# Performance work log

Hardware: AMD Instinct MI355X
Metric: run time of the kernel (lower is better)

Reference implementation:

```python
import jax, jax.numpy as jnp
import numpy as np

B = 512
IN_CORES = 12      # input_eff_capsules = 3072/256
N_PRIM = 12        # num_primary_capsules
N_PAR = 10         # num_parent_capsules
RFPC = 4           # receptive fields per capsule = 256/64
RF = 64            # receptive field size
CAP = 256          # capsule size
P_CONN = 0.2


def setup_inputs() -> dict:
    key = jax.random.key(0)
    ks = jax.random.split(key, 16)
    x = jax.random.uniform(ks[0], (B, 32, 32, 3), dtype=jnp.float32)
    # sparse 0/1 routing tensors (fixed Bernoulli(p) connectivity, stored as float params)
    C1 = jax.random.bernoulli(ks[1], P_CONN, (IN_CORES, RFPC, N_PRIM, RFPC)).astype(jnp.float32)
    C_skip = jax.random.bernoulli(ks[2], P_CONN, (IN_CORES, RFPC, N_PAR, RFPC)).astype(jnp.float32)
    C2 = jax.random.bernoulli(ks[3], P_CONN, (N_PRIM, RFPC, N_PAR, RFPC)).astype(jnp.float32)
    # per-receptive-field linear weights of the capsule layers
    s = 1.0 / np.sqrt(RF)
    W1 = jax.random.normal(ks[4], (N_PRIM, RFPC, RF, RF), dtype=jnp.float32) * s
    b1 = jnp.zeros((N_PRIM, RFPC, RF), dtype=jnp.float32)
    W2 = jax.random.normal(ks[5], (N_PAR, RFPC, RF, RF), dtype=jnp.float32) * s
    b2 = jnp.zeros((N_PAR, RFPC, RF), dtype=jnp.float32)
    # reconstruction MLP: 2560 -> 5000 -> 4000 -> 3072
    Wr1 = jax.random.normal(ks[6], (2560, 5000), dtype=jnp.float32) * (1.0 / np.sqrt(2560))
    br1 = jnp.zeros((5000,), dtype=jnp.float32)
    Wr2 = jax.random.normal(ks[7], (5000, 4000), dtype=jnp.float32) * (1.0 / np.sqrt(5000))
    br2 = jnp.zeros((4000,), dtype=jnp.float32)
    Wr3 = jax.random.normal(ks[8], (4000, 3072), dtype=jnp.float32) * (1.0 / np.sqrt(4000))
    br3 = jnp.zeros((3072,), dtype=jnp.float32)
    return {"x": x, "C1": C1, "W1": W1, "b1": b1, "C_skip": C_skip,
            "C2": C2, "W2": W2, "b2": b2,
            "Wr1": Wr1, "br1": br1, "Wr2": Wr2, "br2": br2, "Wr3": Wr3, "br3": br3}


def _caps_layer(x_flat, C, W, b):
    # x_flat: (B, in_cores*RFPC*RF); C: (in_cores, RFPC, out_caps, RFPC)
    bsz = x_flat.shape[0]
    in_cores = C.shape[0]
    xr = x_flat.reshape(bsz, in_cores, RFPC, RF)
    routed = jnp.einsum('ijkl,bijm->bklm', C, xr)          # (B, out_caps, RFPC, RF)
    out = jax.nn.relu(jnp.einsum('bklm,klmn->bkln', routed, W) + b)
    return out.reshape(bsz, -1)


def reference(x, C1, W1, b1, C_skip, C2, W2, b2, Wr1, br1, Wr2, br2, Wr3, br3):
    bsz = x.shape[0]
    # spatial_block_reshape: pure reshapes -> flatten
    x_flat = x.reshape(bsz, -1)                             # (B, 3072)
    # primary capsule layer
    x_prim = _caps_layer(x_flat, C1, W1, b1)                # (B, 3072)
    # skip connection: sparse routing einsum input->parent
    xr = x_prim.reshape(bsz, IN_CORES, RFPC, RF)
    x_skip = jnp.einsum('ijkl,bijm->bklm', C_skip, xr).reshape(bsz, -1)  # (B, 2560)
    # parent capsule layer + skip
    x_sum = x_skip + _caps_layer(x_prim, C2, W2, b2)        # (B, 2560)
    # top-1 capsule mask by norm
    norms = jnp.linalg.norm(x_sum.reshape(bsz, N_PAR, CAP), axis=-1)  # (B, 10)
    active = jnp.argmax(norms, axis=-1)                     # (B,)
    cap_id = jnp.arange(N_PAR * CAP) // CAP                 # (2560,)
    mask = (cap_id[None, :] == active[:, None]).astype(x_sum.dtype)
    x_recon = mask * x_sum
    # reconstruction MLP
    h = jax.nn.relu(x_recon @ Wr1 + br1)
    h = jax.nn.relu(h @ Wr2 + br2)
    out = jax.nn.sigmoid(h @ Wr3 + br3)                     # (B, 3072)
    return (out, x_sum)
```

## Files before the change

### kernel.cpp

```cpp
#include <hip/hip_runtime.h>
#include <math.h>


#define BATCH 512
#define OUT0_SZ (512*3072)

typedef __attribute__((ext_vector_type(8))) short short8;
typedef __attribute__((ext_vector_type(4))) float f32x4;

__device__ inline unsigned short f2bf(float f) {
    union { float f; unsigned u; } v; v.f = f;
    unsigned r = v.u + 0x7fffu + ((v.u >> 16) & 1u);
    return (unsigned short)(r >> 16);
}
__device__ inline float bf2f(unsigned int hi16) {
    union { unsigned u; float f; } v; v.u = hi16 << 16; return v.f;
}

#define GLD16(g, l) __builtin_amdgcn_global_load_lds( \
    (const __attribute__((address_space(1))) unsigned int*)(g), \
    (__attribute__((address_space(3))) unsigned int*)(l), 16, 0, 0)

struct CTJob {
    const float* W; unsigned short* Wt;
    int Kr, Nr, Kp, k0, n0;
};

__device__ inline CTJob ct_resolve(int bid,
    const float* Wr1, unsigned short* Wt1,
    const float* Wr2, unsigned short* Wt2,
    const float* Wr3, unsigned short* Wt3,
    const float* W1,  unsigned short* W1t,
    const float* W2,  unsigned short* W2t)
{
    CTJob j;
    int ktiles, rem;
    if (bid < 3200)       { j.W = Wr1; j.Wt = Wt1; j.Kr = 2560; j.Nr = 5000; j.Kp = 2560; ktiles = 40; rem = bid; }
    else if (bid < 8320)  { j.W = Wr2; j.Wt = Wt2; j.Kr = 5000; j.Nr = 4000; j.Kp = 5120; ktiles = 80; rem = bid - 3200; }
    else if (bid < 11392) { j.W = Wr3; j.Wt = Wt3; j.Kr = 4000; j.Nr = 3072; j.Kp = 4096; ktiles = 64; rem = bid - 8320; }
    else if (bid < 11440) { int kl = bid - 11392; j.W = W1 + (size_t)kl * 4096; j.Wt = W1t + (size_t)kl * 4096;
                            j.Kr = 64; j.Nr = 64; j.Kp = 64; ktiles = 1; rem = 0; }
    else                  { int kl = bid - 11440; j.W = W2 + (size_t)kl * 4096; j.Wt = W2t + (size_t)kl * 4096;
                            j.Kr = 64; j.Nr = 64; j.Kp = 64; ktiles = 1; rem = 0; }
    j.k0 = (rem % ktiles) * 64;
    j.n0 = (rem / ktiles) * 64;
    return j;
}

__device__ inline void ct_load(const CTJob& j, int tid, float4* v) {
    int kr = tid >> 4;
    int nc = (tid & 15) * 4;
    #pragma unroll
    for (int p = 0; p < 4; ++p) {
        int k = j.k0 + kr + p * 16;
        float4 vv = make_float4(0.f, 0.f, 0.f, 0.f);
        if (k < j.Kr) {
            if (j.n0 + nc + 3 < j.Nr) {
                vv = *(const float4*)&j.W[(size_t)k * j.Nr + j.n0 + nc];
            } else {
                float tmp[4] = {0.f, 0.f, 0.f, 0.f};
                #pragma unroll
                for (int jj = 0; jj < 4; ++jj)
                    if (j.n0 + nc + jj < j.Nr) tmp[jj] = j.W[(size_t)k * j.Nr + j.n0 + nc + jj];
                vv = make_float4(tmp[0], tmp[1], tmp[2], tmp[3]);
            }
        }
        v[p] = vv;
    }
}

__device__ inline void ct_stlds(float* t, int tid, const float4* v) {
    int kr = tid >> 4;
    int nc = (tid & 15) * 4;
    #pragma unroll
    for (int p = 0; p < 4; ++p) {
        float* row = &t[(kr + p * 16) * 65 + nc];
        row[0] = v[p].x; row[1] = v[p].y; row[2] = v[p].z; row[3] = v[p].w;
    }
}

__device__ inline void ct_pack(const CTJob& j, const float* t, int tid) {
    int nr = tid >> 2;
    int kc = (tid & 3) * 16;
    unsigned int u[8];
    #pragma unroll
    for (int jj = 0; jj < 8; ++jj) {
        float v0 = t[(kc + 2 * jj)     * 65 + nr];
        float v1 = t[(kc + 2 * jj + 1) * 65 + nr];
        u[jj] = (unsigned int)f2bf(v0) | ((unsigned int)f2bf(v1) << 16);
    }
    unsigned int* dst = (unsigned int*)&j.Wt[(size_t)(j.n0 + nr) * j.Kp + j.k0 + kc];
    *(uint4*)(dst)     = make_uint4(u[0], u[1], u[2], u[3]);
    *(uint4*)(dst + 4) = make_uint4(u[4], u[5], u[6], u[7]);
}

__global__ __launch_bounds__(256) void convT_all(
    const float* __restrict__ Wr1, unsigned short* __restrict__ Wt1,
    const float* __restrict__ Wr2, unsigned short* __restrict__ Wt2,
    const float* __restrict__ Wr3, unsigned short* __restrict__ Wt3,
    const float* __restrict__ W1,  unsigned short* __restrict__ W1t,
    const float* __restrict__ W2,  unsigned short* __restrict__ W2t)
{
    __shared__ float t[2][64 * 65];
    int tid = threadIdx.x;
    int tbase = blockIdx.x * 4;

    CTJob jc = ct_resolve(tbase, Wr1, Wt1, Wr2, Wt2, Wr3, Wt3, W1, W1t, W2, W2t);
    float4 v[4];
    ct_load(jc, tid, v);
    ct_stlds(t[0], tid, v);
    __syncthreads();

    #pragma unroll
    for (int i = 0; i < 4; ++i) {
        CTJob jn;
        float4 vn[4];
        if (i < 3) {
            jn = ct_resolve(tbase + i + 1, Wr1, Wt1, Wr2, Wt2, Wr3, Wt3, W1, W1t, W2, W2t);
            ct_load(jn, tid, vn);
        }
        ct_pack(jc, t[i & 1], tid);
        if (i < 3) {
            ct_stlds(t[(i + 1) & 1], tid, vn);
            jc = jn;
        }
        __syncthreads();
    }
}

__global__ __launch_bounds__(256) void caps_gemm1(
    const float* __restrict__ x, const float* __restrict__ C1,
    const unsigned short* __restrict__ W1t, const float* __restrict__ b1,
    unsigned short* __restrict__ xp)
{
    __shared__ __align__(16) unsigned short As[128 * 72];
    __shared__ __align__(16) unsigned short Bs[64 * 72];
    __shared__ float Csh[48];
    int kl = blockIdx.x;
    int bm = blockIdx.y * 128;
    int tid = threadIdx.x;
    int w = tid >> 6, lane = tid & 63, q = lane >> 4, r16 = lane & 15;
    int wm = (w >> 1) * 64, wn = (w & 1) * 32;

    if (tid < 48) Csh[tid] = C1[tid * 48 + kl];
    {
        const uint4* src = (const uint4*)(W1t + (size_t)kl * 4096);
        #pragma unroll
        for (int p = 0; p < 2; ++p) {
            int c = tid + p * 256;
            int row = c >> 3, cq = c & 7;
            *(uint4*)&Bs[row * 72 + cq * 8] = src[c];
        }
    }
    __syncthreads();

    int arow = tid >> 1, ah = (tid & 1) * 32;
    float accp[32];
    #pragma unroll
    for (int i = 0; i < 32; ++i) accp[i] = 0.f;
    const float* xrow = x + (size_t)(bm + arow) * 3072 + ah;
    for (int ij = 0; ij < 48; ++ij) {
        float c = Csh[ij];
        if (c != 0.f) {
            const float4* p4 = (const float4*)(xrow + ij * 64);
            #pragma unroll
            for (int cc = 0; cc < 8; ++cc) {
                float4 v = p4[cc];
                accp[cc * 4 + 0] = fmaf(c, v.x, accp[cc * 4 + 0]);
                accp[cc * 4 + 1] = fmaf(c, v.y, accp[cc * 4 + 1]);
                accp[cc * 4 + 2] = fmaf(c, v.z, accp[cc * 4 + 2]);
                accp[cc * 4 + 3] = fmaf(c, v.w, accp[cc * 4 + 3]);
            }
        }
    }
    {
        unsigned short* dst = &As[arow * 72 + ah];
        #pragma unroll
        for (int cc = 0; cc < 4; ++cc) {
            unsigned int u[4];
            #pragma unroll
            for (int j = 0; j < 4; ++j)
                u[j] = (unsigned int)f2bf(accp[cc * 8 + 2 * j]) |
                       ((unsigned int)f2bf(accp[cc * 8 + 2 * j + 1]) << 16);
            *(uint4*)&dst[cc * 8] = make_uint4(u[0], u[1], u[2], u[3]);
        }
    }
    __syncthreads();

    f32x4 acc[4][2];
    #pragma unroll
    for (int i = 0; i < 4; ++i)
        #pragma unroll
        for (int j = 0; j < 2; ++j) acc[i][j] = (f32x4)0.f;
    #pragma unroll
    for (int ks = 0; ks < 2; ++ks) {
        short8 a[4], b[2];
        #pragma unroll
        for (int mt = 0; mt < 4; ++mt)
            a[mt] = *(const short8*)&As[(wm + mt * 16 + r16) * 72 + ks * 32 + q * 8];
        #pragma unroll
        for (int nt = 0; nt < 2; ++nt)
            b[nt] = *(const short8*)&Bs[(wn + nt * 16 + r16) * 72 + ks * 32 + q * 8];
        #pragma unroll
        for (int mt = 0; mt < 4; ++mt)
            #pragma unroll
            for (int nt = 0; nt < 2; ++nt)
                acc[mt][nt] = __builtin_amdgcn_mfma_f32_16x16x32_bf16(a[mt], b[nt], acc[mt][nt], 0, 0, 0);
    }

    #pragma unroll
    for (int mt = 0; mt < 4; ++mt) {
        #pragma unroll
        for (int nt = 0; nt < 2; ++nt) {
            int n = wn + nt * 16 + r16;
            float bv = b1[kl * 64 + n];
            #pragma unroll
            for (int reg = 0; reg < 4; ++reg) {
                int row = bm + wm + mt * 16 + q * 4 + reg;
                xp[(size_t)row * 3072 + kl * 64 + n] = f2bf(fmaxf(acc[mt][nt][reg] + bv, 0.f));
            }
        }
    }
}

__global__ __launch_bounds__(256) void caps_gemm2(
    const unsigned short* __restrict__ xp, const float* __restrict__ Cs,
    const float* __restrict__ C2, const unsigned short* __restrict__ W2t,
    const float* __restrict__ b2, float* __restrict__ xsum,
    float* __restrict__ part8)
{
    __shared__ __align__(16) unsigned short As[128 * 72];
    __shared__ __align__(16) unsigned short Bs[64 * 72];
    __shared__ __align__(16) float Sk[128 * 68];
    __shared__ float C2sh[48], Cssh[48];
    int kl = blockIdx.x;
    int bm = blockIdx.y * 128;
    int tid = threadIdx.x;
    int w = tid >> 6, lane = tid & 63, q = lane >> 4, r16 = lane & 15;
    int wm = (w >> 1) * 64, wn = (w & 1) * 32;
    int half = w & 1;

    if (tid < 48) { C2sh[tid] = C2[tid * 40 + kl]; Cssh[tid] = Cs[tid * 40 + kl]; }
    {
        const uint4* src = (const uint4*)(W2t + (size_t)kl * 4096);
        #pragma unroll
        for (int p = 0; p < 2; ++p) {
            int c = tid + p * 256;
            int row = c >> 3, cq = c & 7;
            *(uint4*)&Bs[row * 72 + cq * 8] = src[c];
        }
    }
    __syncthreads();

    int arow = tid >> 1, ah = (tid & 1) * 32;
    float accp[32], skp[32];
    #pragma unroll
    for (int i = 0; i < 32; ++i) { accp[i] = 0.f; skp[i] = 0.f; }
    const unsigned short* xprow = xp + (size_t)(bm + arow) * 3072 + ah;
    for (int ij = 0; ij < 48; ++ij) {
        float c2 = C2sh[ij], cs = Cssh[ij];
        if (c2 != 0.f || cs != 0.f) {
            const uint4* p4 = (const uint4*)(xprow + ij * 64);
            #pragma unroll
            for (int cc = 0; cc < 4; ++cc) {
                uint4 v = p4[cc];
                unsigned int uu[4] = {v.x, v.y, v.z, v.w};
                #pragma unroll
                for (int j = 0; j < 4; ++j) {
                    float lo = bf2f(uu[j] & 0xffffu);
                    float hi = bf2f(uu[j] >> 16);
                    int idx = cc * 8 + 2 * j;
                    accp[idx]     = fmaf(c2, lo, accp[idx]);
                    accp[idx + 1] = fmaf(c2, hi, accp[idx + 1]);
                    skp[idx]      = fmaf(cs, lo, skp[idx]);
                    skp[idx + 1]  = fmaf(cs, hi, skp[idx + 1]);
                }
            }
        }
    }
    {
        unsigned short* dst = &As[arow * 72 + ah];
        #pragma unroll
        for (int cc = 0; cc < 4; ++cc) {
            unsigned int u[4];
            #pragma unroll
            for (int j = 0; j < 4; ++j)
                u[j] = (unsigned int)f2bf(accp[cc * 8 + 2 * j]) |
                       ((unsigned int)f2bf(accp[cc * 8 + 2 * j + 1]) << 16);
            *(uint4*)&dst[cc * 8] = make_uint4(u[0], u[1], u[2], u[3]);
        }
        float* sdst = &Sk[arow * 68 + ah];
        #pragma unroll
        for (int cc = 0; cc < 8; ++cc)
            *(float4*)&sdst[cc * 4] = make_float4(skp[cc*4], skp[cc*4+1], skp[cc*4+2], skp[cc*4+3]);
    }
    __syncthreads();

    f32x4 acc[4][2];
    #pragma unroll
    for (int i = 0; i < 4; ++i)
        #pragma unroll
        for (int j = 0; j < 2; ++j) acc[i][j] = (f32x4)0.f;
    #pragma unroll
    for (int ks = 0; ks < 2; ++ks) {
        short8 a[4], b[2];
        #pragma unroll
        for (int mt = 0; mt < 4; ++mt)
            a[mt] = *(const short8*)&As[(wm + mt * 16 + r16) * 72 + ks * 32 + q * 8];
        #pragma unroll
        for (int nt = 0; nt < 2; ++nt)
            b[nt] = *(const short8*)&Bs[(wn + nt * 16 + r16) * 72 + ks * 32 + q * 8];
        #pragma unroll
        for (int mt = 0; mt < 4; ++mt)
            #pragma unroll
            for (int nt = 0; nt < 2; ++nt)
                acc[mt][nt] = __builtin_amdgcn_mfma_f32_16x16x32_bf16(a[mt], b[nt], acc[mt][nt], 0, 0, 0);
    }

    #pragma unroll
    for (int mt = 0; mt < 4; ++mt) {
        float sreg[4] = {0.f, 0.f, 0.f, 0.f};
        #pragma unroll
        for (int nt = 0; nt < 2; ++nt) {
            int n = wn + nt * 16 + r16;
            float bv = b2[kl * 64 + n];
            #pragma unroll
            for (int reg = 0; reg < 4; ++reg) {
                int lr = wm + mt * 16 + q * 4 + reg;
                float v = Sk[lr * 68 + n] + fmaxf(acc[mt][nt][reg] + bv, 0.f);
                xsum[(size_t)(bm + lr) * 2560 + kl * 64 + n] = v;
                sreg[reg] += v * v;
            }
        }
        #pragma unroll
        for (int reg = 0; reg < 4; ++reg) {
            float s = sreg[reg];
            s += __shfl_xor(s, 1); s += __shfl_xor(s, 2);
            s += __shfl_xor(s, 4); s += __shfl_xor(s, 8);
            if (r16 == 0) {
                int row = bm + wm + mt * 16 + q * 4 + reg;
                part8[(size_t)row * 80 + kl * 2 + half] = s;
            }
        }
    }
}

__global__ __launch_bounds__(256) void mask_kernel(
    const float* __restrict__ xs, const float* __restrict__ part8,
    unsigned short* __restrict__ xrec, int* __restrict__ active)
{
    int b = blockIdx.x;
    int tid = threadIdx.x;
    __shared__ float norms[10];
    __shared__ int act_sh;
    if (tid < 10) {
        float s = 0.f;
        #pragma unroll
        for (int j = 0; j < 8; ++j) s += part8[(size_t)b * 80 + tid * 8 + j];
        norms[tid] = s;
    }
    __syncthreads();
    if (tid == 0) {
        int best = 0; float bn = -1.f;
        #pragma unroll
        for (int k = 0; k < 10; ++k)
            if (norms[k] > bn) { bn = norms[k]; best = k; }
        act_sh = best;
        active[b] = best;
    }
    __syncthreads();
    int act = act_sh;
    int idx = act * 256 + tid;
    xrec[(size_t)b * 2560 + idx] = f2bf(xs[(size_t)b * 2560 + idx]);
}

__global__ __launch_bounds__(512) void bucket_kernel(
    const int* __restrict__ active, int* __restrict__ perm,
    int4* __restrict__ slots)
{
    __shared__ int cnt[10], pos[10];
    int tid = threadIdx.x;
    if (tid < 10) cnt[tid] = 0;
    __syncthreads();
    int a = active[tid];
    atomicAdd(&cnt[a], 1);
    __syncthreads();
    if (tid == 0) {
        int o = 0, s = 0;
        for (int g = 0; g < 10; ++g) {
            pos[g] = o;
            int mg = cnt[g];
            for (int t0 = 0; t0 < mg; t0 += 64)
                slots[s++] = make_int4(g, o + t0, min(64, mg - t0), 0);
            o += mg;
        }
        for (; s < 18; ++s) slots[s] = make_int4(0, 0, 0, 0);
    }
    __syncthreads();
    int r = atomicAdd(&pos[a], 1);
    perm[r] = tid;
}

__global__ __launch_bounds__(256) void gemm_l1(
    const unsigned short* __restrict__ xrec, const int* __restrict__ perm,
    const int4* __restrict__ slots, const unsigned short* __restrict__ Wt1,
    const float* __restrict__ br1, unsigned short* __restrict__ h1)
{
    int4 s = slots[blockIdx.y];
    if (s.z == 0) return;
    int g = s.x, mstart = s.y, mval = s.z;
    int bn = blockIdx.x * 128;
    int tid = threadIdx.x;

    __shared__ __align__(16) unsigned short As[64 * 32];
    __shared__ __align__(16) unsigned short Bs[128 * 32];
    __shared__ int rows[64];
    if (tid < 64) rows[tid] = perm[mstart + min(tid, mval - 1)];
    __syncthreads();

    int w = tid >> 6, lane = tid & 63;
    int wm = (w >> 1) * 32, wn = (w & 1) * 64;
    int q = lane >> 4, r16 = lane & 15;
    int srow = tid >> 2, skq = tid & 3;

    f32x4 acc[2][4];
    #pragma unroll
    for (int i = 0; i < 2; ++i)
        #pragma unroll
        for (int j = 0; j < 4; ++j) acc[i][j] = (f32x4)0.f;

    int arow = rows[srow];
    const unsigned short* ga = xrec + (size_t)arow * 2560 + g * 256 + skq * 8;
    const unsigned short* gb = Wt1 + (size_t)(bn + srow) * 2560 + g * 256 + skq * 8;

    for (int kk = 0; kk < 256; kk += 32) {
        GLD16(ga + kk, &As[tid * 8]);
        GLD16(gb + kk, &Bs[tid * 8]);
        GLD16(gb + kk + (size_t)64 * 2560, &Bs[(tid + 256) * 8]);
        __syncthreads();

        short8 a[2], b[4];
        #pragma unroll
        for (int mt = 0; mt < 2; ++mt)
            a[mt] = *(const short8*)&As[(wm + mt * 16 + r16) * 32 + q * 8];
        #pragma unroll
        for (int nt = 0; nt < 4; ++nt)
            b[nt] = *(const short8*)&Bs[(wn + nt * 16 + r16) * 32 + q * 8];
        #pragma unroll
        for (int mt = 0; mt < 2; ++mt)
            #pragma unroll
            for (int nt = 0; nt < 4; ++nt)
                acc[mt][nt] = __builtin_amdgcn_mfma_f32_16x16x32_bf16(a[mt], b[nt], acc[mt][nt], 0, 0, 0);
        __syncthreads();
    }

    #pragma unroll
    for (int mt = 0; mt < 2; ++mt) {
        #pragma unroll
        for (int nt = 0; nt < 4; ++nt) {
            int n = bn + wn + nt * 16 + r16;
            float bv = (n < 5000) ? br1[n] : 0.f;
            #pragma unroll
            for (int reg = 0; reg < 4; ++reg) {
                int lm = wm + mt * 16 + q * 4 + reg;
                if (lm < mval)
                    h1[(size_t)(mstart + lm) * 5120 + n] =
                        f2bf(fmaxf(acc[mt][nt][reg] + bv, 0.f));
            }
        }
    }
}

#define SPLITK 4
__global__ __launch_bounds__(256) void gemm_splitk(
    const unsigned short* __restrict__ A, int ldA,
    const unsigned short* __restrict__ Bt, int ldB,
    float* __restrict__ P, int Np, int kper)
{
    __shared__ __align__(16) unsigned short As[64 * 32];
    __shared__ __align__(16) unsigned short Bs[128 * 32];

    int tid = threadIdx.x;
    int bn = blockIdx.x * 128;
    int bm = blockIdx.y * 64;
    int kz = blockIdx.z * kper;

    int w = tid >> 6, lane = tid & 63;
    int wm = (w >> 1) * 32, wn = (w & 1) * 64;
    int q = lane >> 4, r16 = lane & 15;

    int srow = tid >> 2, skq = tid & 3;

    f32x4 acc[2][4];
    #pragma unroll
    for (int i = 0; i < 2; ++i)
        #pragma unroll
        for (int j = 0; j < 4; ++j) acc[i][j] = (f32x4)0.f;

    for (int kk = 0; kk < kper; kk += 32) {
        int k0 = kz + kk;
        const unsigned short* ga = A + (size_t)(bm + srow) * ldA + k0 + skq * 8;
        GLD16(ga, &As[tid * 8]);
        const unsigned short* gb = Bt + (size_t)(bn + srow) * ldB + k0 + skq * 8;
        GLD16(gb, &Bs[tid * 8]);
        GLD16(gb + (size_t)64 * ldB, &Bs[(tid + 256) * 8]);
        __syncthreads();

        short8 a[2], b[4];
        #pragma unroll
        for (int mt = 0; mt < 2; ++mt)
            a[mt] = *(const short8*)&As[(wm + mt * 16 + r16) * 32 + q * 8];
        #pragma unroll
        for (int nt = 0; nt < 4; ++nt)
            b[nt] = *(const short8*)&Bs[(wn + nt * 16 + r16) * 32 + q * 8];
        #pragma unroll
        for (int mt = 0; mt < 2; ++mt)
            #pragma unroll
            for (int nt = 0; nt < 4; ++nt)
                acc[mt][nt] = __builtin_amdgcn_mfma_f32_16x16x32_bf16(a[mt], b[nt], acc[mt][nt], 0, 0, 0);
        __syncthreads();
    }

    float* Pz = P + (size_t)blockIdx.z * 512 * Np;
    #pragma unroll
    for (int mt = 0; mt < 2; ++mt) {
        #pragma unroll
        for (int nt = 0; nt < 4; ++nt) {
            int cn = bn + wn + nt * 16 + r16;
            #pragma unroll
            for (int reg = 0; reg < 4; ++reg) {
                int cm = bm + wm + mt * 16 + q * 4 + reg;
                Pz[(size_t)cm * Np + cn] = acc[mt][nt][reg];
            }
        }
    }
}

template<int MODE>
__global__ __launch_bounds__(256) void combine_kernel(
    const float* __restrict__ P, const float* __restrict__ bias,
    void* __restrict__ out, int Np, int N_real, const int* __restrict__ perm)
{
    int gid = blockIdx.x * 256 + threadIdx.x;
    int n0 = (gid * 4) % Np;
    int m  = (gid * 4) / Np;
    size_t MN = (size_t)512 * Np;
    const float* p = P + (size_t)m * Np + n0;
    f32x4 s = *(const f32x4*)p;
    s += *(const f32x4*)(p + MN);
    s += *(const f32x4*)(p + 2 * MN);
    s += *(const f32x4*)(p + 3 * MN);
    f32x4 bv = (n0 < N_real) ? *(const f32x4*)(bias + n0) : (f32x4)0.f;
    s += bv;
    if (MODE == 0) {
        unsigned int lo = (unsigned int)f2bf(fmaxf(s[0], 0.f)) | ((unsigned int)f2bf(fmaxf(s[1], 0.f)) << 16);
        unsigned int hi = (unsigned int)f2bf(fmaxf(s[2], 0.f)) | ((unsigned int)f2bf(fmaxf(s[3], 0.f)) << 16);
        *(uint2*)((unsigned short*)out + (size_t)m * Np + n0) = make_uint2(lo, hi);
    } else {
        int row = perm[m];
        f32x4 v;
        v[0] = 1.f / (1.f + expf(-s[0]));
        v[1] = 1.f / (1.f + expf(-s[1]));
        v[2] = 1.f / (1.f + expf(-s[2]));
        v[3] = 1.f / (1.f + expf(-s[3]));
        *(f32x4*)((float*)out + (size_t)row * Np + n0) = v;
    }
}

extern "C" void kernel_launch(void* const* d_in, const int* in_sizes, int n_in,
                              void* d_out, int out_size, void* d_ws, size_t ws_size,
                              hipStream_t stream) {
    const float* x   = (const float*)d_in[0];
    const float* C1  = (const float*)d_in[1];
    const float* W1  = (const float*)d_in[2];
    const float* b1  = (const float*)d_in[3];
    const float* Cs  = (const float*)d_in[4];
    const float* C2  = (const float*)d_in[5];
    const float* W2  = (const float*)d_in[6];
    const float* b2  = (const float*)d_in[7];
    const float* Wr1 = (const float*)d_in[8];
    const float* br1 = (const float*)d_in[9];
    const float* Wr2 = (const float*)d_in[10];
    const float* br2 = (const float*)d_in[11];
    const float* Wr3 = (const float*)d_in[12];
    const float* br3 = (const float*)d_in[13];

    float* out = (float*)d_out;
    float* out0     = out;
    float* xsum_out = out + OUT0_SZ;

    char* base = (char*)d_ws;
    unsigned short* xrec  = (unsigned short*)(base);
    unsigned short* h1    = (unsigned short*)(base +   2621440);
    unsigned short* h2    = (unsigned short*)(base +   7864320);
    unsigned short* Wt1   = (unsigned short*)(base +  12058624);
    unsigned short* Wt2   = (unsigned short*)(base +  38273024);
    unsigned short* Wt3   = (unsigned short*)(base +  80216064);
    float*          Pbuf  = (float*)(base + 105381888);
    unsigned short* xp    = (unsigned short*)(base + 147324928);
    unsigned short* W1t   = (unsigned short*)(base + 150470656);
    unsigned short* W2t   = (unsigned short*)(base + 150863872);
    float*          part8 = (float*)(base + 151191552);
    int*  active = (int*)(base + 105381888 + 33554432);
    int*  perm   = active + 512;
    int4* slots  = (int4*)(perm + 512);

    convT_all<<<2870, 256, 0, stream>>>(Wr1, Wt1, Wr2, Wt2, Wr3, Wt3,
                                        W1, W1t, W2, W2t);

    caps_gemm1<<<dim3(48, 4), 256, 0, stream>>>(x, C1, W1t, b1, xp);
    caps_gemm2<<<dim3(40, 4), 256, 0, stream>>>(xp, Cs, C2, W2t, b2, xsum_out, part8);
    mask_kernel<<<BATCH, 256, 0, stream>>>(xsum_out, part8, xrec, active);
    bucket_kernel<<<1, 512, 0, stream>>>(active, perm, slots);

    gemm_l1<<<dim3(5120 / 128, 18), 256, 0, stream>>>(xrec, perm, slots, Wt1, br1, h1);

    gemm_splitk<<<dim3(4096 / 128, 8, SPLITK), 256, 0, stream>>>(h1, 5120, Wt2, 5120, Pbuf, 4096, 5120 / SPLITK);
    combine_kernel<0><<<512 * 4096 / 1024, 256, 0, stream>>>(Pbuf, br2, h2, 4096, 4000, nullptr);

    gemm_splitk<<<dim3(3072 / 128, 8, SPLITK), 256, 0, stream>>>(h2, 4096, Wt3, 4096, Pbuf, 3072, 4096 / SPLITK);
    combine_kernel<1><<<512 * 3072 / 1024, 256, 0, stream>>>(Pbuf, br3, out0, 3072, 3072, perm);
}
```

Before: 384.5 us.

## Interleave weight conversion tiles as guest blocks inside downstream kernels

Removes the standalone big weight transpose/convert kernel. Its tile jobs are split across the pipeline kernels as extra guest blocks, so each weight matrix is converted just before the GEMM that needs it, overlapping conversion with the small capsule/mask stages. It also pads leading dimensions (e.g. 2576, 5136, 4112) to avoid LDS and cache channel conflicts, and drops the skip-value smem staging by writing through global xsum. The cost is larger grids with divergent block roles and a correctness dependence on the guest-block scheduling order. Each weight's conversion must finish in a kernel launched before its consumer, and the guestBase ranges appear to satisfy this.

```diff
diff --git a/kernel.cpp b/kernel.cpp
--- a/kernel.cpp
+++ b/kernel.cpp
@@ -4,6 +4,16 @@
 
 #define BATCH 512
 #define OUT0_SZ (512*3072)
+
+#define KP1 2576
+#define KP2 5136
+#define KP3 4112
+#define LD_XREC 2576
+#define LD_H1 5136
+#define LD_H2 4112
+#define LDP2 4224
+#define LDP3 3200
+#define SPLITK 4
 
 typedef __attribute__((ext_vector_type(8))) short short8;
 typedef __attribute__((ext_vector_type(4))) float f32x4;
@@ -21,123 +31,111 @@
     (const __attribute__((address_space(1))) unsigned int*)(g), \
     (__attribute__((address_space(3))) unsigned int*)(l), 16, 0, 0)
 
-struct CTJob {
+#define GUEST_SMEM 16640
+
+#define CONV_PARAMS const float* __restrict__ cWr1, unsigned short* __restrict__ cWt1, \
+    const float* __restrict__ cWr2, unsigned short* __restrict__ cWt2, \
+    const float* __restrict__ cWr3, unsigned short* __restrict__ cWt3
+
+__device__ void conv_guest(int t, char* smem, CONV_PARAMS)
+{
+    float* sh = (float*)smem;
     const float* W; unsigned short* Wt;
-    int Kr, Nr, Kp, k0, n0;
-};
-
-__device__ inline CTJob ct_resolve(int bid,
-    const float* Wr1, unsigned short* Wt1,
-    const float* Wr2, unsigned short* Wt2,
-    const float* Wr3, unsigned short* Wt3,
-    const float* W1,  unsigned short* W1t,
-    const float* W2,  unsigned short* W2t)
-{
-    CTJob j;
-    int ktiles, rem;
-    if (bid < 3200)       { j.W = Wr1; j.Wt = Wt1; j.Kr = 2560; j.Nr = 5000; j.Kp = 2560; ktiles = 40; rem = bid; }
-    else if (bid < 8320)  { j.W = Wr2; j.Wt = Wt2; j.Kr = 5000; j.Nr = 4000; j.Kp = 5120; ktiles = 80; rem = bid - 3200; }
-    else if (bid < 11392) { j.W = Wr3; j.Wt = Wt3; j.Kr = 4000; j.Nr = 3072; j.Kp = 4096; ktiles = 64; rem = bid - 8320; }
-    else if (bid < 11440) { int kl = bid - 11392; j.W = W1 + (size_t)kl * 4096; j.Wt = W1t + (size_t)kl * 4096;
-                            j.Kr = 64; j.Nr = 64; j.Kp = 64; ktiles = 1; rem = 0; }
-    else                  { int kl = bid - 11440; j.W = W2 + (size_t)kl * 4096; j.Wt = W2t + (size_t)kl * 4096;
-                            j.Kr = 64; j.Nr = 64; j.Kp = 64; ktiles = 1; rem = 0; }
-    j.k0 = (rem % ktiles) * 64;
-    j.n0 = (rem / ktiles) * 64;
-    return j;
-}
-
-__device__ inline void ct_load(const CTJob& j, int tid, float4* v) {
-    int kr = tid >> 4;
-    int nc = (tid & 15) * 4;
+    int Kr, Nr, Kp, ktiles, rem;
+    if (t < 3200)      { W = cWr1; Wt = cWt1; Kr = 2560; Nr = 5000; Kp = KP1; ktiles = 40; rem = t; }
+    else if (t < 8320) { W = cWr2; Wt = cWt2; Kr = 5000; Nr = 4000; Kp = KP2; ktiles = 80; rem = t - 3200; }
+    else               { W = cWr3; Wt = cWt3; Kr = 4000; Nr = 3072; Kp = KP3; ktiles = 64; rem = t - 8320; }
+    int k0 = (rem % ktiles) * 64;
+    int n0 = (rem / ktiles) * 64;
+    int tid = threadIdx.x;
+
+    {
+        int kr = tid >> 4;
+        int nc = (tid & 15) * 4;
+        #pragma unroll
+        for (int p = 0; p < 4; ++p) {
+            int k = k0 + kr + p * 16;
+            float4 v = make_float4(0.f, 0.f, 0.f, 0.f);
+            if (k < Kr) {
+                if (n0 + nc + 3 < Nr) {
+                    v = *(const float4*)&W[(size_t)k * Nr + n0 + nc];
+                } else {
+                    float tmp[4] = {0.f, 0.f, 0.f, 0.f};
+                    #pragma unroll
+                    for (int j = 0; j < 4; ++j)
+                        if (n0 + nc + j < Nr) tmp[j] = W[(size_t)k * Nr + n0 + nc + j];
+                    v = make_float4(tmp[0], tmp[1], tmp[2], tmp[3]);
+                }
+            }
+            float* row = &sh[(kr + p * 16) * 65 + nc];
+            row[0] = v.x; row[1] = v.y; row[2] = v.z; row[3] = v.w;
+        }
+    }
+    __syncthreads();
+    {
+        int nr = tid >> 2;
+        int kc = (tid & 3) * 16;
+        unsigned int u[8];
+        #pragma unroll
+        for (int j = 0; j < 8; ++j) {
+            float v0 = sh[(kc + 2 * j)     * 65 + nr];
+            float v1 = sh[(kc + 2 * j + 1) * 65 + nr];
+            u[j] = (unsigned int)f2bf(v0) | ((unsigned int)f2bf(v1) << 16);
+        }
+        unsigned int* dst = (unsigned int*)&Wt[(size_t)(n0 + nr) * Kp + k0 + kc];
+        *(uint4*)(dst)     = make_uint4(u[0], u[1], u[2], u[3]);
+        *(uint4*)(dst + 4) = make_uint4(u[4], u[5], u[6], u[7]);
+    }
+}
+
+__global__ __launch_bounds__(256) void conv_small(
+    const float* __restrict__ W1, unsigned short* __restrict__ W1t,
+    const float* __restrict__ W2, unsigned short* __restrict__ W2t)
+{
+    __shared__ __align__(16) float sh[64 * 65];
+    int bid = blockIdx.x;
+    const float* W; unsigned short* Wt;
+    if (bid < 48) { W = W1 + (size_t)bid * 4096; Wt = W1t + (size_t)bid * 4096; }
+    else          { W = W2 + (size_t)(bid - 48) * 4096; Wt = W2t + (size_t)(bid - 48) * 4096; }
+    int tid = threadIdx.x;
+    int kr = tid >> 4, nc = (tid & 15) * 4;
     #pragma unroll
     for (int p = 0; p < 4; ++p) {
-        int k = j.k0 + kr + p * 16;
-        float4 vv = make_float4(0.f, 0.f, 0.f, 0.f);
-        if (k < j.Kr) {
-            if (j.n0 + nc + 3 < j.Nr) {
-                vv = *(const float4*)&j.W[(size_t)k * j.Nr + j.n0 + nc];
-            } else {
-                float tmp[4] = {0.f, 0.f, 0.f, 0.f};
-                #pragma unroll
-                for (int jj = 0; jj < 4; ++jj)
-                    if (j.n0 + nc + jj < j.Nr) tmp[jj] = j.W[(size_t)k * j.Nr + j.n0 + nc + jj];
-                vv = make_float4(tmp[0], tmp[1], tmp[2], tmp[3]);
-            }
-        }
-        v[p] = vv;
-    }
-}
-
-__device__ inline void ct_stlds(float* t, int tid, const float4* v) {
-    int kr = tid >> 4;
-    int nc = (tid & 15) * 4;
-    #pragma unroll
-    for (int p = 0; p < 4; ++p) {
-        float* row = &t[(kr + p * 16) * 65 + nc];
-        row[0] = v[p].x; row[1] = v[p].y; row[2] = v[p].z; row[3] = v[p].w;
-    }
-}
-
-__device__ inline void ct_pack(const CTJob& j, const float* t, int tid) {
-    int nr = tid >> 2;
-    int kc = (tid & 3) * 16;
+        float4 v = *(const float4*)&W[(size_t)(kr + p * 16) * 64 + nc];
+        float* row = &sh[(kr + p * 16) * 65 + nc];
+        row[0] = v.x; row[1] = v.y; row[2] = v.z; row[3] = v.w;
+    }
+    __syncthreads();
+    int nr = tid >> 2, kc = (tid & 3) * 16;
     unsigned int u[8];
     #pragma unroll
-    for (int jj = 0; jj < 8; ++jj) {
-        float v0 = t[(kc + 2 * jj)     * 65 + nr];
-        float v1 = t[(kc + 2 * jj + 1) * 65 + nr];
-        u[jj] = (unsigned int)f2bf(v0) | ((unsigned int)f2bf(v1) << 16);
-    }
-    unsigned int* dst = (unsigned int*)&j.Wt[(size_t)(j.n0 + nr) * j.Kp + j.k0 + kc];
+    for (int j = 0; j < 8; ++j) {
+        float v0 = sh[(kc + 2 * j)     * 65 + nr];
+        float v1 = sh[(kc + 2 * j + 1) * 65 + nr];
+        u[j] = (unsigned int)f2bf(v0) | ((unsigned int)f2bf(v1) << 16);
+    }
+    unsigned int* dst = (unsigned int*)&Wt[(size_t)nr * 64 + kc];
     *(uint4*)(dst)     = make_uint4(u[0], u[1], u[2], u[3]);
     *(uint4*)(dst + 4) = make_uint4(u[4], u[5], u[6], u[7]);
 }
 
-__global__ __launch_bounds__(256) void convT_all(
-    const float* __restrict__ Wr1, unsigned short* __restrict__ Wt1,
-    const float* __restrict__ Wr2, unsigned short* __restrict__ Wt2,
-    const float* __restrict__ Wr3, unsigned short* __restrict__ Wt3,
-    const float* __restrict__ W1,  unsigned short* __restrict__ W1t,
-    const float* __restrict__ W2,  unsigned short* __restrict__ W2t)
-{
-    __shared__ float t[2][64 * 65];
-    int tid = threadIdx.x;
-    int tbase = blockIdx.x * 4;
-
-    CTJob jc = ct_resolve(tbase, Wr1, Wt1, Wr2, Wt2, Wr3, Wt3, W1, W1t, W2, W2t);
-    float4 v[4];
-    ct_load(jc, tid, v);
-    ct_stlds(t[0], tid, v);
-    __syncthreads();
-
-    #pragma unroll
-    for (int i = 0; i < 4; ++i) {
-        CTJob jn;
-        float4 vn[4];
-        if (i < 3) {
-            jn = ct_resolve(tbase + i + 1, Wr1, Wt1, Wr2, Wt2, Wr3, Wt3, W1, W1t, W2, W2t);
-            ct_load(jn, tid, vn);
-        }
-        ct_pack(jc, t[i & 1], tid);
-        if (i < 3) {
-            ct_stlds(t[(i + 1) & 1], tid, vn);
-            jc = jn;
-        }
-        __syncthreads();
-    }
-}
-
-__global__ __launch_bounds__(256) void caps_gemm1(
+__global__ __launch_bounds__(256) void caps_gemm1_f(
     const float* __restrict__ x, const float* __restrict__ C1,
     const unsigned short* __restrict__ W1t, const float* __restrict__ b1,
-    unsigned short* __restrict__ xp)
-{
-    __shared__ __align__(16) unsigned short As[128 * 72];
-    __shared__ __align__(16) unsigned short Bs[64 * 72];
-    __shared__ float Csh[48];
-    int kl = blockIdx.x;
-    int bm = blockIdx.y * 128;
+    unsigned short* __restrict__ xp, int hostBlocks, int guestBase,
+    CONV_PARAMS)
+{
+    __shared__ __align__(16) char smem[27840];
+    if ((int)blockIdx.x >= hostBlocks) {
+        conv_guest(guestBase + blockIdx.x - hostBlocks, smem, cWr1, cWt1, cWr2, cWt2, cWr3, cWt3);
+        return;
+    }
+    unsigned short* As = (unsigned short*)smem;
+    unsigned short* Bs = (unsigned short*)(smem + 18432);
+    float* Csh = (float*)(smem + 27648);
+
+    int kl = blockIdx.x % 48;
+    int bm = (blockIdx.x / 48) * 128;
     int tid = threadIdx.x;
     int w = tid >> 6, lane = tid & 63, q = lane >> 4, r16 = lane & 15;
     int wm = (w >> 1) * 64, wn = (w & 1) * 32;
@@ -223,18 +221,25 @@
     }
 }
 
-__global__ __launch_bounds__(256) void caps_gemm2(
+__global__ __launch_bounds__(256) void caps_gemm2_f(
     const unsigned short* __restrict__ xp, const float* __restrict__ Cs,
     const float* __restrict__ C2, const unsigned short* __restrict__ W2t,
     const float* __restrict__ b2, float* __restrict__ xsum,
-    float* __restrict__ part8)
-{
-    __shared__ __align__(16) unsigned short As[128 * 72];
-    __shared__ __align__(16) unsigned short Bs[64 * 72];
-    __shared__ __align__(16) float Sk[128 * 68];
-    __shared__ float C2sh[48], Cssh[48];
-    int kl = blockIdx.x;
-    int bm = blockIdx.y * 128;
+    float* __restrict__ part8, int hostBlocks, int guestBase,
+    CONV_PARAMS)
+{
+    __shared__ __align__(16) char smem[28032];
+    if ((int)blockIdx.x >= hostBlocks) {
+        conv_guest(guestBase + blockIdx.x - hostBlocks, smem, cWr1, cWt1, cWr2, cWt2, cWr3, cWt3);
+        return;
+    }
+    unsigned short* As = (unsigned short*)smem;
+    unsigned short* Bs = (unsigned short*)(smem + 18432);
+    float* C2sh = (float*)(smem + 27648);
+    float* Cssh = (float*)(smem + 27840);
+
+    int kl = blockIdx.x % 40;
+    int bm = (blockIdx.x / 40) * 128;
     int tid = threadIdx.x;
     int w = tid >> 6, lane = tid & 63, q = lane >> 4, r16 = lane & 15;
     int wm = (w >> 1) * 64, wn = (w & 1) * 32;
@@ -289,10 +294,10 @@
                        ((unsigned int)f2bf(accp[cc * 8 + 2 * j + 1]) << 16);
             *(uint4*)&dst[cc * 8] = make_uint4(u[0], u[1], u[2], u[3]);
         }
-        float* sdst = &Sk[arow * 68 + ah];
+        float* sx = xsum + (size_t)(bm + arow) * 2560 + kl * 64 + ah;
         #pragma unroll
         for (int cc = 0; cc < 8; ++cc)
-            *(float4*)&sdst[cc * 4] = make_float4(skp[cc*4], skp[cc*4+1], skp[cc*4+2], skp[cc*4+3]);
+            *(float4*)&sx[cc * 4] = make_float4(skp[cc*4], skp[cc*4+1], skp[cc*4+2], skp[cc*4+3]);
     }
     __syncthreads();
 
@@ -327,8 +332,9 @@
             #pragma unroll
             for (int reg = 0; reg < 4; ++reg) {
                 int lr = wm + mt * 16 + q * 4 + reg;
-                float v = Sk[lr * 68 + n] + fmaxf(acc[mt][nt][reg] + bv, 0.f);
-                xsum[(size_t)(bm + lr) * 2560 + kl * 64 + n] = v;
+                size_t xi = (size_t)(bm + lr) * 2560 + kl * 64 + n;
+                float v = xsum[xi] + fmaxf(acc[mt][nt][reg] + bv, 0.f);
+                xsum[xi] = v;
                 sreg[reg] += v * v;
             }
         }
@@ -345,14 +351,20 @@
     }
 }
 
-__global__ __launch_bounds__(256) void mask_kernel(
+__global__ __launch_bounds__(256) void mask_f(
     const float* __restrict__ xs, const float* __restrict__ part8,
-    unsigned short* __restrict__ xrec, int* __restrict__ active)
-{
+    unsigned short* __restrict__ xrec, int* __restrict__ active,
+    int hostBlocks, int guestBase, CONV_PARAMS)
+{
+    __shared__ __align__(16) char smem[GUEST_SMEM + 64];
+    if ((int)blockIdx.x >= hostBlocks) {
+        conv_guest(guestBase + blockIdx.x - hostBlocks, smem, cWr1, cWt1, cWr2, cWt2, cWr3, cWt3);
+        return;
+    }
+    float* norms = (float*)smem;
+    int* actp = (int*)(smem + 40);
     int b = blockIdx.x;
     int tid = threadIdx.x;
-    __shared__ float norms[10];
-    __shared__ int act_sh;
     if (tid < 10) {
         float s = 0.f;
         #pragma unroll
@@ -365,25 +377,32 @@
         #pragma unroll
         for (int k = 0; k < 10; ++k)
             if (norms[k] > bn) { bn = norms[k]; best = k; }
-        act_sh = best;
+        *actp = best;
         active[b] = best;
     }
     __syncthreads();
-    int act = act_sh;
+    int act = *actp;
     int idx = act * 256 + tid;
-    xrec[(size_t)b * 2560 + idx] = f2bf(xs[(size_t)b * 2560 + idx]);
-}
-
-__global__ __launch_bounds__(512) void bucket_kernel(
+    xrec[(size_t)b * LD_XREC + idx] = f2bf(xs[(size_t)b * 2560 + idx]);
+}
+
+__global__ __launch_bounds__(256) void bucket_f(
     const int* __restrict__ active, int* __restrict__ perm,
-    int4* __restrict__ slots)
-{
-    __shared__ int cnt[10], pos[10];
+    int4* __restrict__ slots, int hostBlocks, int guestBase, CONV_PARAMS)
+{
+    __shared__ __align__(16) char smem[GUEST_SMEM + 128];
+    if ((int)blockIdx.x >= hostBlocks) {
+        conv_guest(guestBase + blockIdx.x - hostBlocks, smem, cWr1, cWt1, cWr2, cWt2, cWr3, cWt3);
+        return;
+    }
+    int* cnt = (int*)smem;
+    int* pos = cnt + 10;
     int tid = threadIdx.x;
     if (tid < 10) cnt[tid] = 0;
     __syncthreads();
-    int a = active[tid];
-    atomicAdd(&cnt[a], 1);
+    int a0 = active[tid], a1 = active[tid + 256];
+    atomicAdd(&cnt[a0], 1);
+    atomicAdd(&cnt[a1], 1);
     __syncthreads();
     if (tid == 0) {
         int o = 0, s = 0;
@@ -397,24 +416,34 @@
         for (; s < 18; ++s) slots[s] = make_int4(0, 0, 0, 0);
     }
     __syncthreads();
-    int r = atomicAdd(&pos[a], 1);
-    perm[r] = tid;
-}
-
-__global__ __launch_bounds__(256) void gemm_l1(
+    int r0 = atomicAdd(&pos[a0], 1);
+    perm[r0] = tid;
+    int r1 = atomicAdd(&pos[a1], 1);
+    perm[r1] = tid + 256;
+}
+
+__global__ __launch_bounds__(256) void gemm_l1_f(
     const unsigned short* __restrict__ xrec, const int* __restrict__ perm,
     const int4* __restrict__ slots, const unsigned short* __restrict__ Wt1,
-    const float* __restrict__ br1, unsigned short* __restrict__ h1)
-{
-    int4 s = slots[blockIdx.y];
+    const float* __restrict__ br1, unsigned short* __restrict__ h1,
+    int hostBlocks, int guestBase, CONV_PARAMS)
+{
+    __shared__ __align__(16) char smem[GUEST_SMEM];
+    if ((int)blockIdx.x >= hostBlocks) {
+        conv_guest(guestBase + blockIdx.x - hostBlocks, smem, cWr1, cWt1, cWr2, cWt2, cWr3, cWt3);
+        return;
+    }
+    unsigned short* As = (unsigned short*)smem;
+    unsigned short* Bs = (unsigned short*)(smem + 4096);
+    int* rows = (int*)(smem + 12288);
+
+    int sy = blockIdx.x % 18;
+    int bn = (blockIdx.x / 18) * 128;
+    int4 s = slots[sy];
     if (s.z == 0) return;
     int g = s.x, mstart = s.y, mval = s.z;
-    int bn = blockIdx.x * 128;
-    int tid = threadIdx.x;
-
-    __shared__ __align__(16) unsigned short As[64 * 32];
-    __shared__ __align__(16) unsigned short Bs[128 * 32];
-    __shared__ int rows[64];
+    int tid = threadIdx.x;
+
     if (tid < 64) rows[tid] = perm[mstart + min(tid, mval - 1)];
     __syncthreads();
 
@@ -430,13 +459,13 @@
         for (int j = 0; j < 4; ++j) acc[i][j] = (f32x4)0.f;
 
     int arow = rows[srow];
-    const unsigned short* ga = xrec + (size_t)arow * 2560 + g * 256 + skq * 8;
-    const unsigned short* gb = Wt1 + (size_t)(bn + srow) * 2560 + g * 256 + skq * 8;
+    const unsigned short* ga = xrec + (size_t)arow * LD_XREC + g * 256 + skq * 8;
+    const unsigned short* gb = Wt1 + (size_t)(bn + srow) * KP1 + g * 256 + skq * 8;
 
     for (int kk = 0; kk < 256; kk += 32) {
         GLD16(ga + kk, &As[tid * 8]);
         GLD16(gb + kk, &Bs[tid * 8]);
-        GLD16(gb + kk + (size_t)64 * 2560, &Bs[(tid + 256) * 8]);
+        GLD16(gb + kk + (size_t)64 * KP1, &Bs[(tid + 256) * 8]);
         __syncthreads();
 
         short8 a[2], b[4];
@@ -464,31 +493,37 @@
             for (int reg = 0; reg < 4; ++reg) {
                 int lm = wm + mt * 16 + q * 4 + reg;
                 if (lm < mval)
-                    h1[(size_t)(mstart + lm) * 5120 + n] =
+                    h1[(size_t)(mstart + lm) * LD_H1 + n] =
                         f2bf(fmaxf(acc[mt][nt][reg] + bv, 0.f));
             }
         }
     }
 }
 
-#define SPLITK 4
-__global__ __launch_bounds__(256) void gemm_splitk(
+__global__ __launch_bounds__(256) void gemm_splitk_f(
     const unsigned short* __restrict__ A, int ldA,
     const unsigned short* __restrict__ Bt, int ldB,
-    float* __restrict__ P, int Np, int kper)
-{
-    __shared__ __align__(16) unsigned short As[64 * 32];
-    __shared__ __align__(16) unsigned short Bs[128 * 32];
-
-    int tid = threadIdx.x;
-    int bn = blockIdx.x * 128;
-    int bm = blockIdx.y * 64;
-    int kz = blockIdx.z * kper;
+    float* __restrict__ P, int ldP, int Np, int kper, int nbx,
+    int hostBlocks, int guestBase, CONV_PARAMS)
+{
+    __shared__ __align__(16) char smem[GUEST_SMEM];
+    if ((int)blockIdx.x >= hostBlocks) {
+        conv_guest(guestBase + blockIdx.x - hostBlocks, smem, cWr1, cWt1, cWr2, cWt2, cWr3, cWt3);
+        return;
+    }
+    unsigned short* As = (unsigned short*)smem;
+    unsigned short* Bs = (unsigned short*)(smem + 4096);
+
+    int tid = threadIdx.x;
+    int bid = blockIdx.x;
+    int bn = (bid % nbx) * 128;
+    int bm = ((bid / nbx) & 7) * 64;
+    int z  = bid / (nbx * 8);
+    int kz = z * kper;
 
     int w = tid >> 6, lane = tid & 63;
     int wm = (w >> 1) * 32, wn = (w & 1) * 64;
     int q = lane >> 4, r16 = lane & 15;
-
     int srow = tid >> 2, skq = tid & 3;
 
     f32x4 acc[2][4];
@@ -521,7 +556,7 @@
         __syncthreads();
     }
 
-    float* Pz = P + (size_t)blockIdx.z * 512 * Np;
+    float* Pz = P + (size_t)z * 512 * ldP;
     #pragma unroll
     for (int mt = 0; mt < 2; ++mt) {
         #pragma unroll
@@ -530,22 +565,28 @@
             #pragma unroll
             for (int reg = 0; reg < 4; ++reg) {
                 int cm = bm + wm + mt * 16 + q * 4 + reg;
-                Pz[(size_t)cm * Np + cn] = acc[mt][nt][reg];
+                Pz[(size_t)cm * ldP + cn] = acc[mt][nt][reg];
             }
         }
     }
 }
 
 template<int MODE>
-__global__ __launch_bounds__(256) void combine_kernel(
-    const float* __restrict__ P, const float* __restrict__ bias,
-    void* __restrict__ out, int Np, int N_real, const int* __restrict__ perm)
-{
+__global__ __launch_bounds__(256) void combine_f(
+    const float* __restrict__ P, int ldP, const float* __restrict__ bias,
+    void* __restrict__ out, int ldO, int Np, int N_real,
+    const int* __restrict__ perm, int hostBlocks, int guestBase, CONV_PARAMS)
+{
+    __shared__ __align__(16) char smem[GUEST_SMEM];
+    if ((int)blockIdx.x >= hostBlocks) {
+        conv_guest(guestBase + blockIdx.x - hostBlocks, smem, cWr1, cWt1, cWr2, cWt2, cWr3, cWt3);
+        return;
+    }
     int gid = blockIdx.x * 256 + threadIdx.x;
     int n0 = (gid * 4) % Np;
     int m  = (gid * 4) / Np;
-    size_t MN = (size_t)512 * Np;
-    const float* p = P + (size_t)m * Np + n0;
+    size_t MN = (size_t)512 * ldP;
+    const float* p = P + (size_t)m * ldP + n0;
     f32x4 s = *(const f32x4*)p;
     s += *(const f32x4*)(p + MN);
     s += *(const f32x4*)(p + 2 * MN);
@@ -555,7 +596,7 @@
     if (MODE == 0) {
         unsigned int lo = (unsigned int)f2bf(fmaxf(s[0], 0.f)) | ((unsigned int)f2bf(fmaxf(s[1], 0.f)) << 16);
         unsigned int hi = (unsigned int)f2bf(fmaxf(s[2], 0.f)) | ((unsigned int)f2bf(fmaxf(s[3], 0.f)) << 16);
-        *(uint2*)((unsigned short*)out + (size_t)m * Np + n0) = make_uint2(lo, hi);
+        *(uint2*)((unsigned short*)out + (size_t)m * ldO + n0) = make_uint2(lo, hi);
     } else {
         int row = perm[m];
         f32x4 v;
@@ -563,7 +604,7 @@
         v[1] = 1.f / (1.f + expf(-s[1]));
         v[2] = 1.f / (1.f + expf(-s[2]));
         v[3] = 1.f / (1.f + expf(-s[3]));
-        *(f32x4*)((float*)out + (size_t)row * Np + n0) = v;
+        *(f32x4*)((float*)out + (size_t)row * ldO + n0) = v;
     }
 }
 
@@ -590,34 +631,35 @@
     float* xsum_out = out + OUT0_SZ;
 
     char* base = (char*)d_ws;
-    unsigned short* xrec  = (unsigned short*)(base);
-    unsigned short* h1    = (unsigned short*)(base +   2621440);
-    unsigned short* h2    = (unsigned short*)(base +   7864320);
-    unsigned short* Wt1   = (unsigned short*)(base +  12058624);
-    unsigned short* Wt2   = (unsigned short*)(base +  38273024);
-    unsigned short* Wt3   = (unsigned short*)(base +  80216064);
-    float*          Pbuf  = (float*)(base + 105381888);
-    unsigned short* xp    = (unsigned short*)(base + 147324928);
-    unsigned short* W1t   = (unsigned short*)(base + 150470656);
-    unsigned short* W2t   = (unsigned short*)(base + 150863872);
-    float*          part8 = (float*)(base + 151191552);
-    int*  active = (int*)(base + 105381888 + 33554432);
+    unsigned short* xrec = (unsigned short*)(base);
+    unsigned short* h1   = (unsigned short*)(base +   2637824);
+    unsigned short* h2   = (unsigned short*)(base +   7897088);
+    unsigned short* Wt1  = (unsigned short*)(base +  12107776);
+    unsigned short* Wt2  = (unsigned short*)(base +  38486016);
+    unsigned short* Wt3  = (unsigned short*)(base +  80560128);
+    float*          Pbuf = (float*)(base + 105824256);
+    unsigned short* xp   = (unsigned short*)(base + 140427264);
+    unsigned short* W1t  = (unsigned short*)(base + 143572992);
+    unsigned short* W2t  = (unsigned short*)(base + 143966208);
+    float*          part8= (float*)(base + 144293888);
+    int*  active = (int*)(base + 144457728);
     int*  perm   = active + 512;
     int4* slots  = (int4*)(perm + 512);
 
-    convT_all<<<2870, 256, 0, stream>>>(Wr1, Wt1, Wr2, Wt2, Wr3, Wt3,
-                                        W1, W1t, W2, W2t);
-
-    caps_gemm1<<<dim3(48, 4), 256, 0, stream>>>(x, C1, W1t, b1, xp);
-    caps_gemm2<<<dim3(40, 4), 256, 0, stream>>>(xp, Cs, C2, W2t, b2, xsum_out, part8);
-    mask_kernel<<<BATCH, 256, 0, stream>>>(xsum_out, part8, xrec, active);
-    bucket_kernel<<<1, 512, 0, stream>>>(active, perm, slots);
-
-    gemm_l1<<<dim3(5120 / 128, 18), 256, 0, stream>>>(xrec, perm, slots, Wt1, br1, h1);
-
-    gemm_splitk<<<dim3(4096 / 128, 8, SPLITK), 256, 0, stream>>>(h1, 5120, Wt2, 5120, Pbuf, 4096, 5120 / SPLITK);
-    combine_kernel<0><<<512 * 4096 / 1024, 256, 0, stream>>>(Pbuf, br2, h2, 4096, 4000, nullptr);
-
-    gemm_splitk<<<dim3(3072 / 128, 8, SPLITK), 256, 0, stream>>>(h2, 4096, Wt3, 4096, Pbuf, 3072, 4096 / SPLITK);
-    combine_kernel<1><<<512 * 3072 / 1024, 256, 0, stream>>>(Pbuf, br3, out0, 3072, 3072, perm);
-}
+    #define CARGS Wr1, Wt1, Wr2, Wt2, Wr3, Wt3
+
+    conv_small<<<88, 256, 0, stream>>>(W1, W1t, W2, W2t);
+
+    caps_gemm1_f<<<192 + 1600, 256, 0, stream>>>(x, C1, W1t, b1, xp, 192, 0, CARGS);
+    caps_gemm2_f<<<160 + 1600, 256, 0, stream>>>(xp, Cs, C2, W2t, b2, xsum_out, part8, 160, 1600, CARGS);
+    mask_f<<<512 + 1300, 256, 0, stream>>>(xsum_out, part8, xrec, active, 512, 3200, CARGS);
+    bucket_f<<<1 + 1300, 256, 0, stream>>>(active, perm, slots, 1, 4500, CARGS);
+
+    gemm_l1_f<<<720 + 2520, 256, 0, stream>>>(xrec, perm, slots, Wt1, br1, h1, 720, 5800, CARGS);
+
+    gemm_splitk_f<<<1024 + 2000, 256, 0, stream>>>(h1, LD_H1, Wt2, KP2, Pbuf, LDP2, 4096, 5120 / SPLITK, 32, 1024, 8320, CARGS);
+    combine_f<0><<<2048 + 1072, 256, 0, stream>>>(Pbuf, LDP2, br2, h2, LD_H2, 4096, 4000, nullptr, 2048, 10320, CARGS);
+
+    gemm_splitk_f<<<768, 256, 0, stream>>>(h2, LD_H2, Wt3, KP3, Pbuf, LDP3, 3072, 4096 / SPLITK, 24, 768, 0, CARGS);
+    combine_f<1><<<1536, 256, 0, stream>>>(Pbuf, LDP3, br3, out0, 3072, 3072, 3072, perm, 1536, 0, CARGS);
+}
```

After: 392.0 us. No clear change (+2.0%).
